# Kernel tuning notes

Measured on AMD Instinct MI355X. Metric: run time of the kernel, lower is better.

The kernel has to match this reference:

```python
import jax, jax.numpy as jnp
import numpy as np

N, E = 50000, 800000
NUM_TYPES = 5
NUM_HEADS = 4
HIDDEN = 32
IN_DIM = 128
NEG_SLOPE = 0.2


def typed_linear(x, types, W):
    # x: [M, in], types: [M] int, W: [T, in, out] -> [M, out]
    out = jnp.zeros((x.shape[0], W.shape[2]), dtype=x.dtype)
    for t in range(W.shape[0]):
        out = out + jnp.where((types == t)[:, None], x @ W[t], jnp.zeros((), x.dtype))
    return out


def setup_inputs() -> dict:
    key = jax.random.key(0)
    ks = jax.random.split(key, 10)
    x = jax.random.normal(ks[0], (N, IN_DIM), dtype=jnp.float32)
    ntype = jax.random.randint(ks[1], (N,), 0, NUM_TYPES)
    etype = jax.random.randint(ks[2], (E,), 0, NUM_TYPES)
    src = jax.random.randint(ks[3], (E,), 0, N)
    dst = jax.random.randint(ks[4], (E,), 0, N)
    sc = 1.0 / np.sqrt(IN_DIM)
    W_typed = jax.random.normal(ks[5], (NUM_TYPES, IN_DIM, HIDDEN * NUM_HEADS), dtype=jnp.float32) * sc
    al_w = jax.random.normal(ks[6], (NUM_TYPES, HIDDEN, HIDDEN), dtype=jnp.float32) * (1.0 / np.sqrt(HIDDEN))
    ar_w = jax.random.normal(ks[7], (NUM_TYPES, HIDDEN, HIDDEN), dtype=jnp.float32) * (1.0 / np.sqrt(HIDDEN))
    W_res = jax.random.normal(ks[8], (IN_DIM, HIDDEN * NUM_HEADS), dtype=jnp.float32) * sc
    b_res = jax.random.normal(ks[9], (HIDDEN * NUM_HEADS,), dtype=jnp.float32) * 0.01
    return {"x": x, "ntype": ntype, "etype": etype, "src": src, "dst": dst,
            "W_typed": W_typed, "al_w": al_w, "ar_w": ar_w, "W_res": W_res, "b_res": b_res}


def reference(x, ntype, etype, src, dst, W_typed, al_w, ar_w, W_res, b_res):
    n = x.shape[0]
    # typed projection W (dropout in the original is applied to `feat` but discarded)
    feat = typed_linear(x, ntype, W_typed)                    # [N, H*D]
    h = feat.reshape(n, NUM_HEADS, HIDDEN)                    # [N, H, D]
    ntype_rep = jnp.repeat(ntype, NUM_HEADS)                  # row n*H+h has node n's type
    h_flat = h.reshape(-1, HIDDEN)
    h_l = typed_linear(h_flat, ntype_rep, al_w).reshape(n, NUM_HEADS, HIDDEN).sum(-1)  # [N, H]
    h_r = typed_linear(h_flat, ntype_rep, ar_w).reshape(n, NUM_HEADS, HIDDEN).sum(-1)  # [N, H]
    e = jax.nn.leaky_relu(h_l[src] + h_r[dst], NEG_SLOPE)     # [E, H]
    # edge softmax grouped by destination node
    m = jax.ops.segment_max(e, dst, num_segments=n)           # [N, H]
    ex = jnp.exp(e - m[dst])
    s = jax.ops.segment_sum(ex, dst, num_segments=n)          # [N, H]
    alpha = ex / s[dst]                                       # [E, H]
    # u_mul_e + sum aggregation
    msg = h[src] * alpha[:, :, None]                          # [E, H, D]
    agg = jax.ops.segment_sum(msg, dst, num_segments=n)       # [N, H, D]
    out = agg.transpose(0, 2, 1).reshape(n, HIDDEN * NUM_HEADS)  # matches permute(0,2,1).view
    out = out + x @ W_res + b_res                             # residual
    return jax.nn.relu(out)                                   # activation
```

## Files before the change

### kernel.cpp

```cpp
#include <hip/hip_runtime.h>
#include <cstdint>
#include <cstddef>

#define IN_DIM 128
#define HID 32
#define NH 4
#define OUT_DIM 128
#define NEG 0.2f
#define NT 5
#define BPT 16
#define NCOLS 272
#define NTILE 17
#define TILE_ELEMS 2048
#define CAPN 50048
#define NPREP 40
#define RSHIFT 7
#define SLOT0 16
#define MAXD 56
#define ABLK 2048
#define CAPB 8192

typedef __attribute__((ext_vector_type(8))) __bf16 bf16x8;
typedef __attribute__((ext_vector_type(4))) float f32x4;

static __device__ __forceinline__ float leaky(float v) { return v > 0.f ? v : NEG * v; }
static __device__ __forceinline__ float blo(unsigned u) { return __uint_as_float(u << 16); }
static __device__ __forceinline__ float bhi(unsigned u) { return __uint_as_float(u & 0xffff0000u); }

__global__ void __launch_bounds__(256) setup_kernel(
        const int* __restrict__ dstp, const int* __restrict__ srcp,
        unsigned* __restrict__ binned, int* __restrict__ gcur, int E, int nba,
        const int* __restrict__ ntype, int* __restrict__ tcur, int* __restrict__ order,
        int N, int nbs,
        const float* __restrict__ Wt, const float* __restrict__ Wres,
        const float* __restrict__ alw, const float* __restrict__ arw,
        __bf16* __restrict__ Whi, __bf16* __restrict__ Wlo) {
    __shared__ unsigned pk[ABLK];
    __shared__ int hist[256], basea[256], cura[256];
    __shared__ float alv[HID], arv[HID];
    int bid = blockIdx.x, tid = threadIdx.x;

    if (bid < nba) {
        hist[tid] = 0;
        cura[tid] = 0;
        __syncthreads();
        int e0 = bid * ABLK;
        int cnt = E - e0;
        if (cnt > ABLK) cnt = ABLK;
        for (int k = tid; k < cnt; k += 256) {
            int d = dstp[e0 + k];
            int s = srcp[e0 + k];
            int bb = d >> 8;
            pk[k] = ((unsigned)bb << 24) | ((unsigned)(d & 255) << 16) | (unsigned)s;
            atomicAdd(&hist[bb], 1);
        }
        __syncthreads();
        if (hist[tid] > 0) basea[tid] = atomicAdd(&gcur[tid], hist[tid]);
        __syncthreads();
        for (int k = tid; k < cnt; k += 256) {
            unsigned p = pk[k];
            int bb = p >> 24;
            int r = atomicAdd(&cura[bb], 1);
            int pos = basea[bb] + r;
            if (pos < CAPB) binned[(size_t)bb * CAPB + pos] = p;
        }
        return;
    }
    bid -= nba;
    if (bid < nbs) {
        if (tid < NT) hist[tid] = 0;
        __syncthreads();
        int gid = bid * 256 + tid;
        int t = -1, rank = 0;
        if (gid < N) {
            t = ntype[gid];
            rank = atomicAdd(&hist[t], 1);
        }
        __syncthreads();
        if (tid < NT && hist[tid] > 0) basea[tid] = atomicAdd(&tcur[tid], hist[tid]);
        __syncthreads();
        if (gid < N) order[t * CAPN + basea[t] + rank] = gid;
        return;
    }
    bid -= nbs;
    {
        int t = bid >> 3, part = bid & 7;
        if (tid < 64) {
            int which = tid >= HID;
            int i = tid & (HID - 1);
            const float* p = (which ? arw : alw) + ((size_t)t * HID + i) * HID;
            float s = 0.f;
            for (int j = 0; j < HID; ++j) s += p[j];
            (which ? arv : alv)[i] = s;
        }
        __syncthreads();
        int end = (part + 1) * 4352;
        for (int idx = part * 4352 + tid; idx < end; idx += 256) {
            int n = idx >> 7, k = idx & 127;
            float w;
            if (n < 128) {
                w = Wt[((size_t)t * IN_DIM + k) * OUT_DIM + n];
            } else if (n < 256) {
                w = Wres[(size_t)k * OUT_DIM + (n - 128)];
            } else if (n < 264) {
                int h = (n - 256) & 3;
                const float* av = (n >= 260) ? arv : alv;
                float s = 0.f;
                for (int i = 0; i < HID; ++i)
                    s += Wt[((size_t)t * IN_DIM + k) * OUT_DIM + h * HID + i] * av[i];
                w = s;
            } else {
                w = 0.f;
            }
            __bf16 hi = (__bf16)w;
            __bf16 lo = (__bf16)(w - (float)hi);
            size_t o = (size_t)(t * NTILE + (n >> 4)) * TILE_ELEMS
                     + (size_t)(((k >> 3) * 16 + (n & 15)) << 3) + (k & 7);
            Whi[o] = hi;
            Wlo[o] = lo;
        }
    }
}

__global__ void __launch_bounds__(256) mega3_kernel(
        const unsigned* __restrict__ binned, const int* __restrict__ gcur,
        char* __restrict__ rec, int N, int nbuck,
        const float* __restrict__ x, const int* __restrict__ order,
        const int* __restrict__ tcur,
        const __bf16* __restrict__ Whi, const __bf16* __restrict__ Wlo,
        const float* __restrict__ bres,
        __bf16* __restrict__ h_bf, float* __restrict__ hl, float* __restrict__ hr,
        float* __restrict__ out) {
    __shared__ bf16x8 lds_hi[256];
    __shared__ bf16x8 lds_lo[256];
    __shared__ int nids_s[BPT];
    __shared__ int lcnt[256];
    int bid = blockIdx.x;
    int q = bid / 17, r17 = bid - q * 17;
    int tid = threadIdx.x;

    if (r17 == 16) {
        if (q >= nbuck) return;
        lcnt[tid] = 0;
        __syncthreads();
        int cnt = gcur[q];
        if (cnt > CAPB) cnt = CAPB;
        const unsigned* bp = binned + (size_t)q * CAPB;
        for (int k = tid; k < cnt; k += 256) {
            unsigned p = bp[k];
            int dl = (p >> 16) & 255;
            int r = atomicAdd(&lcnt[dl], 1);
            if (r < MAXD)
                *(unsigned short*)(rec + (((size_t)(q << 8) + dl) << RSHIFT) + SLOT0 + 2 * r)
                    = (unsigned short)(p & 0xffffu);
        }
        __syncthreads();
        int node = (q << 8) + tid;
        if (node < N) {
            int c = lcnt[tid];
            if (c > MAXD) c = MAXD;
            *(int*)(rec + ((size_t)node << RSHIFT)) = c;
        }
        return;
    }

    int b = 16 * q + r17;
    int t = -1, lb = 0, cthis = 0;
    {
        int pbl = 0;
        for (int tt = 0; tt < NT; ++tt) {
            int c = tcur[tt];
            int ntt = (c + BPT - 1) >> 4;
            if (b < pbl + ntt) { t = tt; lb = b - pbl; cthis = c; break; }
            pbl += ntt;
        }
    }
    if (t < 0) return;
    int base = lb * BPT;

    {
        int row = tid >> 4, c = tid & 15;
        int li = base + row;
        int nd = (li < cthis) ? order[t * CAPN + li] : -1;
        if (tid < BPT) nids_s[tid] = (base + tid < cthis) ? order[t * CAPN + base + tid] : -1;
        float4 v0 = make_float4(0.f, 0.f, 0.f, 0.f), v1 = v0;
        if (nd >= 0) {
            const float4* xr = (const float4*)(x + (size_t)nd * IN_DIM + c * 8);
            v0 = xr[0];
            v1 = xr[1];
        }
        float f[8] = {v0.x, v0.y, v0.z, v0.w, v1.x, v1.y, v1.z, v1.w};
        bf16x8 hv, lv;
#pragma unroll
        for (int j = 0; j < 8; ++j) {
            __bf16 h = (__bf16)f[j];
            hv[j] = h;
            lv[j] = (__bf16)(f[j] - (float)h);
        }
        lds_hi[c * 16 + row] = hv;
        lds_lo[c * 16 + row] = lv;
    }
    __syncthreads();

    int w = tid >> 6, lane = tid & 63;
    int lr = lane & 15, lg = lane >> 4;
    bool w3 = (w == 3);

    const __bf16* Wbh = Whi + (size_t)t * NTILE * TILE_ELEMS;
    const __bf16* Wbl = Wlo + (size_t)t * NTILE * TILE_ELEMS;

    f32x4 acc[5];
#pragma unroll
    for (int nt = 0; nt < 5; ++nt) acc[nt] = (f32x4)0.f;

#pragma unroll
    for (int ks = 0; ks < 4; ++ks) {
        int ai = ks * 64 + lg * 16 + lr;
        size_t ao = (size_t)ai << 3;
        bf16x8 ah = lds_hi[ai];
        bf16x8 al = lds_lo[ai];
#pragma unroll
        for (int nt = 0; nt < 5; ++nt) {
            if (nt == 4 && !w3) continue;
            int ng = (nt < 4) ? (nt * 4 + w) : 16;
            bf16x8 bh = *(const bf16x8*)(Wbh + (size_t)ng * TILE_ELEMS + ao);
            acc[nt] = __builtin_amdgcn_mfma_f32_16x16x32_bf16(al, bh, acc[nt], 0, 0, 0);
            acc[nt] = __builtin_amdgcn_mfma_f32_16x16x32_bf16(ah, bh, acc[nt], 0, 0, 0);
            if (nt == 4) {
                bf16x8 bl = *(const bf16x8*)(Wbl + (size_t)16 * TILE_ELEMS + ao);
                acc[4] = __builtin_amdgcn_mfma_f32_16x16x32_bf16(ah, bl, acc[4], 0, 0, 0);
            }
        }
    }

    int nids[4];
#pragma unroll
    for (int r = 0; r < 4; ++r) nids[r] = nids_s[lg * 4 + r];

#pragma unroll
    for (int nt = 0; nt < 5; ++nt) {
        if (nt == 4 && !w3) continue;
        int ng = (nt < 4) ? (nt * 4 + w) : 16;
        int col = ng * 16 + lr;
        float bb = (col >= 128 && col < 256) ? bres[col - 128] : 0.f;
#pragma unroll
        for (int r = 0; r < 4; ++r) {
            int nid = nids[r];
            if (nid < 0) continue;
            float v = acc[nt][r];
            if (col < 128) {
                h_bf[(size_t)nid * OUT_DIM + col] = (__bf16)v;
            } else if (col < 256) {
                out[(size_t)nid * OUT_DIM + (col - 128)] = v + bb;
            } else if (col < 260) {
                hl[nid * NH + (col - 256)] = v;
            } else if (col < 264) {
                hr[nid * NH + (col - 260)] = v;
            }
        }
    }
}

__global__ void agg_kernel(const char* __restrict__ rec,
                           const float* __restrict__ hlf,
                           const float4* __restrict__ hr4, const __bf16* __restrict__ h_bf,
                           float* __restrict__ out, int n_nodes) {
    int gid = blockIdx.x * 256 + threadIdx.x;
    int n = gid >> 4;
    if (n >= n_nodes) return;
    int l = threadIdx.x & 15;
    int myh = l >> 2;
    const char* rp = rec + ((size_t)n << RSHIFT);
    int deg = *(const int*)rp;
    const unsigned short* ss = (const unsigned short*)(rp + SLOT0);
    float acc[8];
#pragma unroll
    for (int m = 0; m < 8; ++m) acc[m] = 0.f;

    if (deg > 0) {
        float4 hv = hr4[n];
        float hrh = myh < 2 ? (myh == 0 ? hv.x : hv.y) : (myh == 2 ? hv.z : hv.w);
        float sw = 0.f;
        int k = 0;
        for (; k + 8 <= deg; k += 8) {
            uint4 sp = *(const uint4*)(ss + k);
            int sv[8];
            sv[0] = sp.x & 0xffff; sv[1] = sp.x >> 16;
            sv[2] = sp.y & 0xffff; sv[3] = sp.y >> 16;
            sv[4] = sp.z & 0xffff; sv[5] = sp.z >> 16;
            sv[6] = sp.w & 0xffff; sv[7] = sp.w >> 16;
            uint4 u[8];
            float e[8];
#pragma unroll
            for (int j = 0; j < 8; ++j) {
                u[j] = *(const uint4*)(h_bf + (size_t)sv[j] * OUT_DIM + l * 8);
                e[j] = hlf[sv[j] * 4 + myh];
            }
#pragma unroll
            for (int j = 0; j < 8; ++j) {
                float wv = __expf(leaky(e[j] + hrh));
                sw += wv;
                acc[0] += wv * blo(u[j].x); acc[1] += wv * bhi(u[j].x);
                acc[2] += wv * blo(u[j].y); acc[3] += wv * bhi(u[j].y);
                acc[4] += wv * blo(u[j].z); acc[5] += wv * bhi(u[j].z);
                acc[6] += wv * blo(u[j].w); acc[7] += wv * bhi(u[j].w);
            }
        }
        for (; k < deg; ++k) {
            int sv0 = ss[k];
            uint4 u0 = *(const uint4*)(h_bf + (size_t)sv0 * OUT_DIM + l * 8);
            float e0 = hlf[sv0 * 4 + myh];
            float wv = __expf(leaky(e0 + hrh));
            sw += wv;
            acc[0] += wv * blo(u0.x); acc[1] += wv * bhi(u0.x);
            acc[2] += wv * blo(u0.y); acc[3] += wv * bhi(u0.y);
            acc[4] += wv * blo(u0.z); acc[5] += wv * bhi(u0.z);
            acc[6] += wv * blo(u0.w); acc[7] += wv * bhi(u0.w);
        }
        float inv_s = 1.f / sw;
#pragma unroll
        for (int m = 0; m < 8; ++m) acc[m] *= inv_s;
    }
    size_t ob = (size_t)n * OUT_DIM;
    int based = (l & 3) << 3;
#pragma unroll
    for (int m = 0; m < 8; ++m) {
        int j = ((based + m) << 2) | myh;
        out[ob + j] = fmaxf(acc[m] + out[ob + j], 0.f);
    }
}

extern "C" void kernel_launch(void* const* d_in, const int* in_sizes, int n_in,
                              void* d_out, int out_size, void* d_ws, size_t ws_size,
                              hipStream_t stream) {
    const float* x     = (const float*)d_in[0];
    const int*   ntype = (const int*)d_in[1];
    const int*   src   = (const int*)d_in[3];
    const int*   dst   = (const int*)d_in[4];
    const float* Wt    = (const float*)d_in[5];
    const float* alw   = (const float*)d_in[6];
    const float* arw   = (const float*)d_in[7];
    const float* Wres  = (const float*)d_in[8];
    const float* bres  = (const float*)d_in[9];
    float* out = (float*)d_out;
    int N = in_sizes[1];
    int E = in_sizes[3];

    char* ws = (char*)d_ws;
    size_t off = 0;
    auto alloc = [&](size_t bytes) -> char* {
        char* p = ws + off;
        off += (bytes + 255) & ~(size_t)255;
        return p;
    };
    __bf16* h_bf       = (__bf16*)alloc((size_t)N * OUT_DIM * 2);
    float*  hl         = (float*)alloc((size_t)N * NH * 4);
    float*  hr         = (float*)alloc((size_t)N * NH * 4);
    int*    order      = (int*)alloc((size_t)NT * CAPN * 4);
    __bf16* Whi        = (__bf16*)alloc((size_t)NT * NTILE * TILE_ELEMS * 2);
    __bf16* Wlo        = (__bf16*)alloc((size_t)NT * NTILE * TILE_ELEMS * 2);
    char*   rec        = (char*)alloc((size_t)N << RSHIFT);
    unsigned* binned   = (unsigned*)alloc((size_t)256 * CAPB * 4);
    char*   zstart     = ws + off;
    int*    gcur       = (int*)alloc(256 * 4);
    int*    tcur       = (int*)alloc(NT * 4);
    size_t  zlen       = (ws + off) - zstart;

    hipMemsetAsync(zstart, 0, zlen, stream);

    int nbs = (N + 255) / 256;
    int nba = (E + ABLK - 1) / ABLK;
    int nbuck = (N + 255) >> 8;

    setup_kernel<<<nba + nbs + NPREP, 256, 0, stream>>>(
        dst, src, binned, gcur, E, nba,
        ntype, tcur, order, N, nbs,
        Wt, Wres, alw, arw, Whi, Wlo);

    int pbmax = (N + BPT - 1) / BPT + NT;
    int qproj = (pbmax + 15) / 16;
    int qmax = qproj > nbuck ? qproj : nbuck;
    mega3_kernel<<<17 * qmax, 256, 0, stream>>>(
        binned, gcur, rec, N, nbuck,
        x, order, tcur, Whi, Wlo, bres, h_bf, hl, hr, out);

    agg_kernel<<<(N * 16 + 255) / 256, 256, 0, stream>>>(rec, hl, (const float4*)hr,
                                                         h_bf, out, N);
}
```

Baseline: 103.5 us.

## Double projection tile to 32 nodes per block and drop low-part MFMAs

The projection blocks now process 32 nodes as two 16-row MFMA sub-tiles, so each weight fragment loaded from global memory feeds two MFMAs. The interleave of projection and bucket blocks is rebalanced to 6:1. For the main output columns, the correction MFMA using the low bf16 part of x is removed, leaving a single bf16 product. This cuts matrix-core work but lowers the accuracy of the h and residual outputs. Doubling the tile also means fewer, larger blocks and more accumulator registers.

```diff
diff --git a/kernel.cpp b/kernel.cpp
--- a/kernel.cpp
+++ b/kernel.cpp
@@ -8,7 +8,7 @@
 #define OUT_DIM 128
 #define NEG 0.2f
 #define NT 5
-#define BPT 16
+#define BPT 32
 #define NCOLS 272
 #define NTILE 17
 #define TILE_ELEMS 2048
@@ -122,7 +122,7 @@
     }
 }
 
-__global__ void __launch_bounds__(256) mega3_kernel(
+__global__ void __launch_bounds__(256) mega4_kernel(
         const unsigned* __restrict__ binned, const int* __restrict__ gcur,
         char* __restrict__ rec, int N, int nbuck,
         const float* __restrict__ x, const int* __restrict__ order,
@@ -131,15 +131,15 @@
         const float* __restrict__ bres,
         __bf16* __restrict__ h_bf, float* __restrict__ hl, float* __restrict__ hr,
         float* __restrict__ out) {
-    __shared__ bf16x8 lds_hi[256];
-    __shared__ bf16x8 lds_lo[256];
+    __shared__ bf16x8 lds_hi[512];
+    __shared__ bf16x8 lds_lo[512];
     __shared__ int nids_s[BPT];
     __shared__ int lcnt[256];
     int bid = blockIdx.x;
-    int q = bid / 17, r17 = bid - q * 17;
+    int q = bid / 7, r7 = bid - q * 7;
     int tid = threadIdx.x;
 
-    if (r17 == 16) {
+    if (r7 == 6) {
         if (q >= nbuck) return;
         lcnt[tid] = 0;
         __syncthreads();
@@ -164,13 +164,13 @@
         return;
     }
 
-    int b = 16 * q + r17;
+    int b = 6 * q + r7;
     int t = -1, lb = 0, cthis = 0;
     {
         int pbl = 0;
         for (int tt = 0; tt < NT; ++tt) {
             int c = tcur[tt];
-            int ntt = (c + BPT - 1) >> 4;
+            int ntt = (c + BPT - 1) >> 5;
             if (b < pbl + ntt) { t = tt; lb = b - pbl; cthis = c; break; }
             pbl += ntt;
         }
@@ -178,11 +178,12 @@
     if (t < 0) return;
     int base = lb * BPT;
 
-    {
-        int row = tid >> 4, c = tid & 15;
+#pragma unroll
+    for (int it = 0; it < 2; ++it) {
+        int idx = tid + it * 256;
+        int row = idx >> 4, c = idx & 15;
         int li = base + row;
         int nd = (li < cthis) ? order[t * CAPN + li] : -1;
-        if (tid < BPT) nids_s[tid] = (base + tid < cthis) ? order[t * CAPN + base + tid] : -1;
         float4 v0 = make_float4(0.f, 0.f, 0.f, 0.f), v1 = v0;
         if (nd >= 0) {
             const float4* xr = (const float4*)(x + (size_t)nd * IN_DIM + c * 8);
@@ -197,9 +198,11 @@
             hv[j] = h;
             lv[j] = (__bf16)(f[j] - (float)h);
         }
-        lds_hi[c * 16 + row] = hv;
-        lds_lo[c * 16 + row] = lv;
-    }
+        int mi = row >> 4, r = row & 15;
+        lds_hi[mi * 256 + c * 16 + r] = hv;
+        lds_lo[mi * 256 + c * 16 + r] = lv;
+    }
+    if (tid < BPT) nids_s[tid] = (base + tid < cthis) ? order[t * CAPN + base + tid] : -1;
     __syncthreads();
 
     int w = tid >> 6, lane = tid & 63;
@@ -209,33 +212,39 @@
     const __bf16* Wbh = Whi + (size_t)t * NTILE * TILE_ELEMS;
     const __bf16* Wbl = Wlo + (size_t)t * NTILE * TILE_ELEMS;
 
-    f32x4 acc[5];
-#pragma unroll
-    for (int nt = 0; nt < 5; ++nt) acc[nt] = (f32x4)0.f;
+    f32x4 acc[2][5];
+#pragma unroll
+    for (int m = 0; m < 2; ++m)
+#pragma unroll
+        for (int nt = 0; nt < 5; ++nt) acc[m][nt] = (f32x4)0.f;
 
 #pragma unroll
     for (int ks = 0; ks < 4; ++ks) {
-        int ai = ks * 64 + lg * 16 + lr;
-        size_t ao = (size_t)ai << 3;
-        bf16x8 ah = lds_hi[ai];
-        bf16x8 al = lds_lo[ai];
-#pragma unroll
-        for (int nt = 0; nt < 5; ++nt) {
-            if (nt == 4 && !w3) continue;
-            int ng = (nt < 4) ? (nt * 4 + w) : 16;
+        int ci = ks * 4 + lg;
+        int fo = ci * 16 + lr;
+        size_t ao = (size_t)fo << 3;
+        bf16x8 ah0 = lds_hi[fo];
+        bf16x8 ah1 = lds_hi[256 + fo];
+#pragma unroll
+        for (int nt = 0; nt < 4; ++nt) {
+            int ng = nt * 4 + w;
             bf16x8 bh = *(const bf16x8*)(Wbh + (size_t)ng * TILE_ELEMS + ao);
-            acc[nt] = __builtin_amdgcn_mfma_f32_16x16x32_bf16(al, bh, acc[nt], 0, 0, 0);
-            acc[nt] = __builtin_amdgcn_mfma_f32_16x16x32_bf16(ah, bh, acc[nt], 0, 0, 0);
-            if (nt == 4) {
-                bf16x8 bl = *(const bf16x8*)(Wbl + (size_t)16 * TILE_ELEMS + ao);
-                acc[4] = __builtin_amdgcn_mfma_f32_16x16x32_bf16(ah, bl, acc[4], 0, 0, 0);
-            }
-        }
-    }
-
-    int nids[4];
-#pragma unroll
-    for (int r = 0; r < 4; ++r) nids[r] = nids_s[lg * 4 + r];
+            acc[0][nt] = __builtin_amdgcn_mfma_f32_16x16x32_bf16(ah0, bh, acc[0][nt], 0, 0, 0);
+            acc[1][nt] = __builtin_amdgcn_mfma_f32_16x16x32_bf16(ah1, bh, acc[1][nt], 0, 0, 0);
+        }
+        if (w3) {
+            bf16x8 al0 = lds_lo[fo];
+            bf16x8 al1 = lds_lo[256 + fo];
+            bf16x8 bh16 = *(const bf16x8*)(Wbh + (size_t)16 * TILE_ELEMS + ao);
+            bf16x8 bl16 = *(const bf16x8*)(Wbl + (size_t)16 * TILE_ELEMS + ao);
+            acc[0][4] = __builtin_amdgcn_mfma_f32_16x16x32_bf16(al0, bh16, acc[0][4], 0, 0, 0);
+            acc[0][4] = __builtin_amdgcn_mfma_f32_16x16x32_bf16(ah0, bl16, acc[0][4], 0, 0, 0);
+            acc[0][4] = __builtin_amdgcn_mfma_f32_16x16x32_bf16(ah0, bh16, acc[0][4], 0, 0, 0);
+            acc[1][4] = __builtin_amdgcn_mfma_f32_16x16x32_bf16(al1, bh16, acc[1][4], 0, 0, 0);
+            acc[1][4] = __builtin_amdgcn_mfma_f32_16x16x32_bf16(ah1, bl16, acc[1][4], 0, 0, 0);
+            acc[1][4] = __builtin_amdgcn_mfma_f32_16x16x32_bf16(ah1, bh16, acc[1][4], 0, 0, 0);
+        }
+    }
 
 #pragma unroll
     for (int nt = 0; nt < 5; ++nt) {
@@ -244,18 +253,21 @@
         int col = ng * 16 + lr;
         float bb = (col >= 128 && col < 256) ? bres[col - 128] : 0.f;
 #pragma unroll
-        for (int r = 0; r < 4; ++r) {
-            int nid = nids[r];
-            if (nid < 0) continue;
-            float v = acc[nt][r];
-            if (col < 128) {
-                h_bf[(size_t)nid * OUT_DIM + col] = (__bf16)v;
-            } else if (col < 256) {
-                out[(size_t)nid * OUT_DIM + (col - 128)] = v + bb;
-            } else if (col < 260) {
-                hl[nid * NH + (col - 256)] = v;
-            } else if (col < 264) {
-                hr[nid * NH + (col - 260)] = v;
+        for (int m = 0; m < 2; ++m) {
+#pragma unroll
+            for (int r = 0; r < 4; ++r) {
+                int nid = nids_s[m * 16 + lg * 4 + r];
+                if (nid < 0) continue;
+                float v = acc[m][nt][r];
+                if (col < 128) {
+                    h_bf[(size_t)nid * OUT_DIM + col] = (__bf16)v;
+                } else if (col < 256) {
+                    out[(size_t)nid * OUT_DIM + (col - 128)] = v + bb;
+                } else if (col < 260) {
+                    hl[nid * NH + (col - 256)] = v;
+                } else if (col < 264) {
+                    hr[nid * NH + (col - 260)] = v;
+                }
             }
         }
     }
@@ -378,9 +390,9 @@
         Wt, Wres, alw, arw, Whi, Wlo);
 
     int pbmax = (N + BPT - 1) / BPT + NT;
-    int qproj = (pbmax + 15) / 16;
+    int qproj = (pbmax + 5) / 6;
     int qmax = qproj > nbuck ? qproj : nbuck;
-    mega3_kernel<<<17 * qmax, 256, 0, stream>>>(
+    mega4_kernel<<<7 * qmax, 256, 0, stream>>>(
         binned, gcur, rec, N, nbuck,
         x, order, tcur, Whi, Wlo, bres, h_bf, hl, hr, out);
 
```

New measurement: 101.0 us (median of 3 runs). 1.02x faster.

## Sort node types locally per 128-node block instead of global type ordering

Applied to the files above, without the earlier changes.

Removes the global per-type node ordering pass and the order buffer. Each projection block now loads 128 contiguous x rows into LDS, bins them by type in shared memory, and runs MFMA tiles per type. The projection is interleaved with the edge-binning blocks in one kernel, and the weight prep and bucket pass B become separate launches. Numerics change too: the lo-part of x is now used only for the hl/hr column tile instead of all columns, cutting MFMA work at some precision cost for h and the residual. This raises the launch count from three to four and leaves partially filled type tiles inside each block.

```diff
diff --git a/kernel.cpp b/kernel.cpp
--- a/kernel.cpp
+++ b/kernel.cpp
@@ -8,17 +8,17 @@
 #define OUT_DIM 128
 #define NEG 0.2f
 #define NT 5
-#define BPT 16
 #define NCOLS 272
 #define NTILE 17
 #define TILE_ELEMS 2048
-#define CAPN 50048
-#define NPREP 40
 #define RSHIFT 7
 #define SLOT0 16
 #define MAXD 56
 #define ABLK 2048
 #define CAPB 8192
+#define PBLK 128
+#define MAXTILE 12
+#define NPREP 80
 
 typedef __attribute__((ext_vector_type(8))) __bf16 bf16x8;
 typedef __attribute__((ext_vector_type(4))) float f32x4;
@@ -27,24 +27,69 @@
 static __device__ __forceinline__ float blo(unsigned u) { return __uint_as_float(u << 16); }
 static __device__ __forceinline__ float bhi(unsigned u) { return __uint_as_float(u & 0xffff0000u); }
 
-__global__ void __launch_bounds__(256) setup_kernel(
-        const int* __restrict__ dstp, const int* __restrict__ srcp,
-        unsigned* __restrict__ binned, int* __restrict__ gcur, int E, int nba,
-        const int* __restrict__ ntype, int* __restrict__ tcur, int* __restrict__ order,
-        int N, int nbs,
+__global__ void __launch_bounds__(256) wprep_kernel(
         const float* __restrict__ Wt, const float* __restrict__ Wres,
         const float* __restrict__ alw, const float* __restrict__ arw,
         __bf16* __restrict__ Whi, __bf16* __restrict__ Wlo) {
-    __shared__ unsigned pk[ABLK];
-    __shared__ int hist[256], basea[256], cura[256];
     __shared__ float alv[HID], arv[HID];
+    int t = blockIdx.x >> 4, part = blockIdx.x & 15;
+    int tid = threadIdx.x;
+    if (tid < 64) {
+        int which = tid >= HID;
+        int i = tid & (HID - 1);
+        const float* p = (which ? arw : alw) + ((size_t)t * HID + i) * HID;
+        float s = 0.f;
+        for (int j = 0; j < HID; ++j) s += p[j];
+        (which ? arv : alv)[i] = s;
+    }
+    __syncthreads();
+    int seg = NCOLS * IN_DIM / 16;
+    int end = (part + 1) * seg;
+    for (int idx = part * seg + tid; idx < end; idx += 256) {
+        int n = idx >> 7, k = idx & 127;
+        float w;
+        if (n < 128) {
+            w = Wt[((size_t)t * IN_DIM + k) * OUT_DIM + n];
+        } else if (n < 256) {
+            w = Wres[(size_t)k * OUT_DIM + (n - 128)];
+        } else if (n < 264) {
+            int h = (n - 256) & 3;
+            const float* av = (n >= 260) ? arv : alv;
+            float s = 0.f;
+            for (int i = 0; i < HID; ++i)
+                s += Wt[((size_t)t * IN_DIM + k) * OUT_DIM + h * HID + i] * av[i];
+            w = s;
+        } else {
+            w = 0.f;
+        }
+        __bf16 hi = (__bf16)w;
+        __bf16 lo = (__bf16)(w - (float)hi);
+        size_t o = (size_t)(t * NTILE + (n >> 4)) * TILE_ELEMS
+                 + (size_t)(((k >> 3) * 16 + (n & 15)) << 3) + (k & 7);
+        Whi[o] = hi;
+        Wlo[o] = lo;
+    }
+}
+
+__global__ void __launch_bounds__(256) mega5_kernel(
+        const int* __restrict__ dstp, const int* __restrict__ srcp,
+        unsigned* __restrict__ binned, int* __restrict__ gcur, int E, int nba,
+        const float* __restrict__ x, const int* __restrict__ ntype, int N,
+        const __bf16* __restrict__ Whi, const __bf16* __restrict__ Wlo,
+        const float* __restrict__ bres,
+        __bf16* __restrict__ h_bf, float* __restrict__ hl, float* __restrict__ hr,
+        float* __restrict__ out) {
     int bid = blockIdx.x, tid = threadIdx.x;
 
-    if (bid < nba) {
+    if (!(bid & 1)) {
+        __shared__ unsigned pk[ABLK];
+        __shared__ int hist[256], basea[256], cura[256];
+        int ab = bid >> 1;
+        if (ab >= nba) return;
         hist[tid] = 0;
         cura[tid] = 0;
         __syncthreads();
-        int e0 = bid * ABLK;
+        int e0 = ab * ABLK;
         int cnt = E - e0;
         if (cnt > ABLK) cnt = ABLK;
         for (int k = tid; k < cnt; k += 256) {
@@ -66,129 +111,35 @@
         }
         return;
     }
-    bid -= nba;
-    if (bid < nbs) {
-        if (tid < NT) hist[tid] = 0;
-        __syncthreads();
-        int gid = bid * 256 + tid;
-        int t = -1, rank = 0;
-        if (gid < N) {
-            t = ntype[gid];
-            rank = atomicAdd(&hist[t], 1);
-        }
-        __syncthreads();
-        if (tid < NT && hist[tid] > 0) basea[tid] = atomicAdd(&tcur[tid], hist[tid]);
-        __syncthreads();
-        if (gid < N) order[t * CAPN + basea[t] + rank] = gid;
-        return;
-    }
-    bid -= nbs;
-    {
-        int t = bid >> 3, part = bid & 7;
-        if (tid < 64) {
-            int which = tid >= HID;
-            int i = tid & (HID - 1);
-            const float* p = (which ? arw : alw) + ((size_t)t * HID + i) * HID;
-            float s = 0.f;
-            for (int j = 0; j < HID; ++j) s += p[j];
-            (which ? arv : alv)[i] = s;
-        }
-        __syncthreads();
-        int end = (part + 1) * 4352;
-        for (int idx = part * 4352 + tid; idx < end; idx += 256) {
-            int n = idx >> 7, k = idx & 127;
-            float w;
-            if (n < 128) {
-                w = Wt[((size_t)t * IN_DIM + k) * OUT_DIM + n];
-            } else if (n < 256) {
-                w = Wres[(size_t)k * OUT_DIM + (n - 128)];
-            } else if (n < 264) {
-                int h = (n - 256) & 3;
-                const float* av = (n >= 260) ? arv : alv;
-                float s = 0.f;
-                for (int i = 0; i < HID; ++i)
-                    s += Wt[((size_t)t * IN_DIM + k) * OUT_DIM + h * HID + i] * av[i];
-                w = s;
-            } else {
-                w = 0.f;
-            }
-            __bf16 hi = (__bf16)w;
-            __bf16 lo = (__bf16)(w - (float)hi);
-            size_t o = (size_t)(t * NTILE + (n >> 4)) * TILE_ELEMS
-                     + (size_t)(((k >> 3) * 16 + (n & 15)) << 3) + (k & 7);
-            Whi[o] = hi;
-            Wlo[o] = lo;
-        }
-    }
-}
-
-__global__ void __launch_bounds__(256) mega3_kernel(
-        const unsigned* __restrict__ binned, const int* __restrict__ gcur,
-        char* __restrict__ rec, int N, int nbuck,
-        const float* __restrict__ x, const int* __restrict__ order,
-        const int* __restrict__ tcur,
-        const __bf16* __restrict__ Whi, const __bf16* __restrict__ Wlo,
-        const float* __restrict__ bres,
-        __bf16* __restrict__ h_bf, float* __restrict__ hl, float* __restrict__ hr,
-        float* __restrict__ out) {
-    __shared__ bf16x8 lds_hi[256];
-    __shared__ bf16x8 lds_lo[256];
-    __shared__ int nids_s[BPT];
-    __shared__ int lcnt[256];
-    int bid = blockIdx.x;
-    int q = bid / 17, r17 = bid - q * 17;
-    int tid = threadIdx.x;
-
-    if (r17 == 16) {
-        if (q >= nbuck) return;
-        lcnt[tid] = 0;
-        __syncthreads();
-        int cnt = gcur[q];
-        if (cnt > CAPB) cnt = CAPB;
-        const unsigned* bp = binned + (size_t)q * CAPB;
-        for (int k = tid; k < cnt; k += 256) {
-            unsigned p = bp[k];
-            int dl = (p >> 16) & 255;
-            int r = atomicAdd(&lcnt[dl], 1);
-            if (r < MAXD)
-                *(unsigned short*)(rec + (((size_t)(q << 8) + dl) << RSHIFT) + SLOT0 + 2 * r)
-                    = (unsigned short)(p & 0xffffu);
-        }
-        __syncthreads();
-        int node = (q << 8) + tid;
-        if (node < N) {
-            int c = lcnt[tid];
-            if (c > MAXD) c = MAXD;
-            *(int*)(rec + ((size_t)node << RSHIFT)) = c;
-        }
-        return;
-    }
-
-    int b = 16 * q + r17;
-    int t = -1, lb = 0, cthis = 0;
-    {
-        int pbl = 0;
-        for (int tt = 0; tt < NT; ++tt) {
-            int c = tcur[tt];
-            int ntt = (c + BPT - 1) >> 4;
-            if (b < pbl + ntt) { t = tt; lb = b - pbl; cthis = c; break; }
-            pbl += ntt;
-        }
-    }
-    if (t < 0) return;
-    int base = lb * BPT;
-
-    {
-        int row = tid >> 4, c = tid & 15;
-        int li = base + row;
-        int nd = (li < cthis) ? order[t * CAPN + li] : -1;
-        if (tid < BPT) nids_s[tid] = (base + tid < cthis) ? order[t * CAPN + base + tid] : -1;
-        float4 v0 = make_float4(0.f, 0.f, 0.f, 0.f), v1 = v0;
-        if (nd >= 0) {
-            const float4* xr = (const float4*)(x + (size_t)nd * IN_DIM + c * 8);
-            v0 = xr[0];
-            v1 = xr[1];
-        }
+
+    __shared__ bf16x8 s_hi[16 * PBLK];
+    __shared__ bf16x8 s_lo[16 * PBLK];
+    __shared__ short nloc[MAXTILE * 16];
+    __shared__ char ttype_s[MAXTILE];
+    __shared__ int thist[NT], tbase_s[NT], tcur_s[NT], s_ntiles;
+    int pb = bid >> 1;
+    int nproj = (N + PBLK - 1) / PBLK;
+    if (pb >= nproj) return;
+    int base = pb * PBLK;
+    int cnt = N - base;
+    if (cnt > PBLK) cnt = PBLK;
+
+    if (tid < NT) { thist[tid] = 0; tcur_s[tid] = 0; }
+    for (int i = tid; i < MAXTILE * 16; i += 256) nloc[i] = -1;
+    __syncthreads();
+
+    int myt = -1;
+    if (tid < cnt) {
+        myt = ntype[base + tid];
+        atomicAdd(&thist[myt], 1);
+    }
+#pragma unroll
+    for (int it = 0; it < 8; ++it) {
+        int idx = tid + it * 256;
+        int lrow = idx >> 4, c = idx & 15;
+        if (lrow >= cnt) continue;
+        const float4* xr = (const float4*)(x + ((size_t)(base + lrow) << 7) + (c << 3));
+        float4 v0 = xr[0], v1 = xr[1];
         float f[8] = {v0.x, v0.y, v0.z, v0.w, v1.x, v1.y, v1.z, v1.w};
         bf16x8 hv, lv;
 #pragma unroll
@@ -197,67 +148,112 @@
             hv[j] = h;
             lv[j] = (__bf16)(f[j] - (float)h);
         }
-        lds_hi[c * 16 + row] = hv;
-        lds_lo[c * 16 + row] = lv;
+        s_hi[c * PBLK + lrow] = hv;
+        s_lo[c * PBLK + lrow] = lv;
+    }
+    __syncthreads();
+    if (tid == 0) {
+        int cpos = 0;
+        for (int t = 0; t < NT; ++t) {
+            tbase_s[t] = cpos;
+            int ntt = (thist[t] + 15) >> 4;
+            for (int k = 0; k < ntt; ++k) ttype_s[(cpos >> 4) + k] = (char)t;
+            cpos += ntt << 4;
+        }
+        s_ntiles = cpos >> 4;
+    }
+    __syncthreads();
+    if (tid < cnt) {
+        int r = atomicAdd(&tcur_s[myt], 1);
+        nloc[tbase_s[myt] + r] = (short)tid;
     }
     __syncthreads();
 
     int w = tid >> 6, lane = tid & 63;
     int lr = lane & 15, lg = lane >> 4;
     bool w3 = (w == 3);
-
-    const __bf16* Wbh = Whi + (size_t)t * NTILE * TILE_ELEMS;
-    const __bf16* Wbl = Wlo + (size_t)t * NTILE * TILE_ELEMS;
-
-    f32x4 acc[5];
-#pragma unroll
-    for (int nt = 0; nt < 5; ++nt) acc[nt] = (f32x4)0.f;
-
-#pragma unroll
-    for (int ks = 0; ks < 4; ++ks) {
-        int ai = ks * 64 + lg * 16 + lr;
-        size_t ao = (size_t)ai << 3;
-        bf16x8 ah = lds_hi[ai];
-        bf16x8 al = lds_lo[ai];
+    int ntiles = s_ntiles;
+
+    for (int mt = 0; mt < ntiles; ++mt) {
+        int t = ttype_s[mt];
+        int alrow = nloc[mt * 16 + lr];
+        int arow = alrow < 0 ? 0 : alrow;
+        const __bf16* Wbh = Whi + (size_t)t * NTILE * TILE_ELEMS;
+        const __bf16* Wbl = Wlo + (size_t)t * NTILE * TILE_ELEMS;
+        f32x4 acc[5];
+#pragma unroll
+        for (int nt = 0; nt < 5; ++nt) acc[nt] = (f32x4)0.f;
+
+#pragma unroll
+        for (int ks = 0; ks < 4; ++ks) {
+            int ci = ks * 4 + lg;
+            bf16x8 ah = s_hi[ci * PBLK + arow];
+            size_t ao = (size_t)((ci << 4) + lr) << 3;
+#pragma unroll
+            for (int nt = 0; nt < 4; ++nt) {
+                bf16x8 bh = *(const bf16x8*)(Wbh + (size_t)(nt * 4 + w) * TILE_ELEMS + ao);
+                acc[nt] = __builtin_amdgcn_mfma_f32_16x16x32_bf16(ah, bh, acc[nt], 0, 0, 0);
+            }
+            if (w3) {
+                bf16x8 al = s_lo[ci * PBLK + arow];
+                bf16x8 bh16 = *(const bf16x8*)(Wbh + (size_t)16 * TILE_ELEMS + ao);
+                bf16x8 bl16 = *(const bf16x8*)(Wbl + (size_t)16 * TILE_ELEMS + ao);
+                acc[4] = __builtin_amdgcn_mfma_f32_16x16x32_bf16(al, bh16, acc[4], 0, 0, 0);
+                acc[4] = __builtin_amdgcn_mfma_f32_16x16x32_bf16(ah, bl16, acc[4], 0, 0, 0);
+                acc[4] = __builtin_amdgcn_mfma_f32_16x16x32_bf16(ah, bh16, acc[4], 0, 0, 0);
+            }
+        }
+
 #pragma unroll
         for (int nt = 0; nt < 5; ++nt) {
             if (nt == 4 && !w3) continue;
             int ng = (nt < 4) ? (nt * 4 + w) : 16;
-            bf16x8 bh = *(const bf16x8*)(Wbh + (size_t)ng * TILE_ELEMS + ao);
-            acc[nt] = __builtin_amdgcn_mfma_f32_16x16x32_bf16(al, bh, acc[nt], 0, 0, 0);
-            acc[nt] = __builtin_amdgcn_mfma_f32_16x16x32_bf16(ah, bh, acc[nt], 0, 0, 0);
-            if (nt == 4) {
-                bf16x8 bl = *(const bf16x8*)(Wbl + (size_t)16 * TILE_ELEMS + ao);
-                acc[4] = __builtin_amdgcn_mfma_f32_16x16x32_bf16(ah, bl, acc[4], 0, 0, 0);
-            }
-        }
-    }
-
-    int nids[4];
-#pragma unroll
-    for (int r = 0; r < 4; ++r) nids[r] = nids_s[lg * 4 + r];
-
-#pragma unroll
-    for (int nt = 0; nt < 5; ++nt) {
-        if (nt == 4 && !w3) continue;
-        int ng = (nt < 4) ? (nt * 4 + w) : 16;
-        int col = ng * 16 + lr;
-        float bb = (col >= 128 && col < 256) ? bres[col - 128] : 0.f;
-#pragma unroll
-        for (int r = 0; r < 4; ++r) {
-            int nid = nids[r];
-            if (nid < 0) continue;
-            float v = acc[nt][r];
-            if (col < 128) {
-                h_bf[(size_t)nid * OUT_DIM + col] = (__bf16)v;
-            } else if (col < 256) {
-                out[(size_t)nid * OUT_DIM + (col - 128)] = v + bb;
-            } else if (col < 260) {
-                hl[nid * NH + (col - 256)] = v;
-            } else if (col < 264) {
-                hr[nid * NH + (col - 260)] = v;
-            }
-        }
+            int col = ng * 16 + lr;
+            float bb = (col >= 128 && col < 256) ? bres[col - 128] : 0.f;
+#pragma unroll
+            for (int r = 0; r < 4; ++r) {
+                int lro = nloc[mt * 16 + lg * 4 + r];
+                if (lro < 0) continue;
+                int nid = base + lro;
+                float v = acc[nt][r];
+                if (col < 128) {
+                    h_bf[(size_t)nid * OUT_DIM + col] = (__bf16)v;
+                } else if (col < 256) {
+                    out[(size_t)nid * OUT_DIM + (col - 128)] = v + bb;
+                } else if (col < 260) {
+                    hl[nid * NH + (col - 256)] = v;
+                } else if (col < 264) {
+                    hr[nid * NH + (col - 260)] = v;
+                }
+            }
+        }
+    }
+}
+
+__global__ void __launch_bounds__(256) passb_kernel(
+        const unsigned* __restrict__ binned, const int* __restrict__ gcur,
+        char* __restrict__ rec, int N) {
+    __shared__ int lcnt[256];
+    int q = blockIdx.x, tid = threadIdx.x;
+    lcnt[tid] = 0;
+    __syncthreads();
+    int cnt = gcur[q];
+    if (cnt > CAPB) cnt = CAPB;
+    const unsigned* bp = binned + (size_t)q * CAPB;
+    for (int k = tid; k < cnt; k += 256) {
+        unsigned p = bp[k];
+        int dl = (p >> 16) & 255;
+        int r = atomicAdd(&lcnt[dl], 1);
+        if (r < MAXD)
+            *(unsigned short*)(rec + (((size_t)(q << 8) + dl) << RSHIFT) + SLOT0 + 2 * r)
+                = (unsigned short)(p & 0xffffu);
+    }
+    __syncthreads();
+    int node = (q << 8) + tid;
+    if (node < N) {
+        int c = lcnt[tid];
+        if (c > MAXD) c = MAXD;
+        *(int*)(rec + ((size_t)node << RSHIFT)) = c;
     }
 }
 
@@ -356,33 +352,29 @@
     __bf16* h_bf       = (__bf16*)alloc((size_t)N * OUT_DIM * 2);
     float*  hl         = (float*)alloc((size_t)N * NH * 4);
     float*  hr         = (float*)alloc((size_t)N * NH * 4);
-    int*    order      = (int*)alloc((size_t)NT * CAPN * 4);
     __bf16* Whi        = (__bf16*)alloc((size_t)NT * NTILE * TILE_ELEMS * 2);
     __bf16* Wlo        = (__bf16*)alloc((size_t)NT * NTILE * TILE_ELEMS * 2);
     char*   rec        = (char*)alloc((size_t)N << RSHIFT);
     unsigned* binned   = (unsigned*)alloc((size_t)256 * CAPB * 4);
     char*   zstart     = ws + off;
     int*    gcur       = (int*)alloc(256 * 4);
-    int*    tcur       = (int*)alloc(NT * 4);
     size_t  zlen       = (ws + off) - zstart;
 
     hipMemsetAsync(zstart, 0, zlen, stream);
 
-    int nbs = (N + 255) / 256;
     int nba = (E + ABLK - 1) / ABLK;
+    int nproj = (N + PBLK - 1) / PBLK;
     int nbuck = (N + 255) >> 8;
 
-    setup_kernel<<<nba + nbs + NPREP, 256, 0, stream>>>(
+    wprep_kernel<<<NPREP, 256, 0, stream>>>(Wt, Wres, alw, arw, Whi, Wlo);
+
+    int qmax = nba > nproj ? nba : nproj;
+    mega5_kernel<<<2 * qmax, 256, 0, stream>>>(
         dst, src, binned, gcur, E, nba,
-        ntype, tcur, order, N, nbs,
-        Wt, Wres, alw, arw, Whi, Wlo);
-
-    int pbmax = (N + BPT - 1) / BPT + NT;
-    int qproj = (pbmax + 15) / 16;
-    int qmax = qproj > nbuck ? qproj : nbuck;
-    mega3_kernel<<<17 * qmax, 256, 0, stream>>>(
-        binned, gcur, rec, N, nbuck,
-        x, order, tcur, Whi, Wlo, bres, h_bf, hl, hr, out);
+        x, ntype, N,
+        Whi, Wlo, bres, h_bf, hl, hr, out);
+
+    passb_kernel<<<nbuck, 256, 0, stream>>>(binned, gcur, rec, N);
 
     agg_kernel<<<(N * 16 + 255) / 256, 256, 0, stream>>>(rec, hl, (const float4*)hr,
                                                          h_bf, out, N);
```

Measured after the change: 153.6 us. +48.5%, slower.
